# Kernel optimization log

Measured on AMD Instinct MI355X. Metric: run time of the kernel, lower is better.

## Reference

```python
import jax, jax.numpy as jnp
import numpy as np

N_NODES = 50000
N_EDGES = 800000
D_IN = 128
D_HID = 128
N_CLASSES = 40


def gcn_conv(h, src, dst, W, b, n_nodes):
    """GCNConv: out = D^{-1/2} (A + I) D^{-1/2} (h @ W) + b, with self-loops."""
    h = h @ W  # [N, F_out]
    loop = jnp.arange(n_nodes, dtype=src.dtype)
    s = jnp.concatenate([src, loop])  # [E + N]
    d = jnp.concatenate([dst, loop])
    deg = jax.ops.segment_sum(jnp.ones_like(d, dtype=h.dtype), d, num_segments=n_nodes)
    dinv = jax.lax.rsqrt(jnp.maximum(deg, 1.0))  # deg >= 1 due to self-loops
    norm = dinv[s] * dinv[d]  # [E + N]
    msgs = h[s] * norm[:, None]  # gather: [E + N, F_out]
    out = jax.ops.segment_sum(msgs, d, num_segments=n_nodes)  # scatter-add
    return out + b


def setup_inputs() -> dict:
    key = jax.random.key(0)
    ks = jax.random.split(key, 12)
    x = jax.random.normal(ks[0], (N_NODES, D_IN), dtype=jnp.float32)
    edge_index = jax.random.randint(ks[1], (2, N_EDGES), 0, N_NODES, dtype=jnp.int64)
    def lin(k, fi, fo):
        s = 1.0 / np.sqrt(fi)
        return jax.random.uniform(k, (fi, fo), jnp.float32, -s, s)
    W_pre = lin(ks[2], D_IN, D_HID)
    b_pre = jnp.zeros((D_HID,), jnp.float32)
    W1 = lin(ks[3], D_HID, D_HID)
    b1 = jnp.zeros((D_HID,), jnp.float32)
    W2 = lin(ks[4], D_HID, D_HID)
    b2 = jnp.zeros((D_HID,), jnp.float32)
    W_post = lin(ks[5], D_HID, N_CLASSES)
    b_post = jnp.zeros((N_CLASSES,), jnp.float32)
    return {"x": x, "edge_index": edge_index, "W_pre": W_pre, "b_pre": b_pre,
            "W1": W1, "b1": b1, "W2": W2, "b2": b2,
            "W_post": W_post, "b_post": b_post}


def reference(x, edge_index, W_pre, b_pre, W1, b1, W2, b2, W_post, b_post):
    src, dst = edge_index[0], edge_index[1]
    n = x.shape[0]
    h = x @ W_pre + b_pre                      # pre-process MLP (Linear)
    h = jax.nn.relu(gcn_conv(h, src, dst, W1, b1, n))   # conv1 + act1
    h = jax.nn.relu(gcn_conv(h, src, dst, W2, b2, n))   # conv2 + act2
    return h @ W_post + b_post                 # post-process MLP (Linear)
```

## Files before the change

### kernel.cpp

```cpp
#include <hip/hip_runtime.h>

#define D 128

typedef short bfrag __attribute__((ext_vector_type(8)));
typedef float f32x4 __attribute__((ext_vector_type(4)));
typedef unsigned uint32;

__device__ inline unsigned short bf16_rne(float x) {
    unsigned u = __float_as_uint(x);
    return (unsigned short)((u + 0x7FFFu + ((u >> 16) & 1u)) >> 16);
}
__device__ inline float bf16_to_f(unsigned short h) {
    return __uint_as_float(((unsigned)h) << 16);
}
__device__ inline unsigned split2p(float x) {
    unsigned short hi = bf16_rne(x);
    unsigned short lo = bf16_rne(x - bf16_to_f(hi));
    return (unsigned)hi | ((unsigned)lo << 16);
}

__device__ inline void unpair_r(uint4 q0, uint4 q1, bfrag& ah, bfrag& al) {
    union { uint32 u[4]; bfrag b; } H, L;
    H.u[0] = __builtin_amdgcn_perm(q0.y, q0.x, 0x05040100u);
    H.u[1] = __builtin_amdgcn_perm(q0.w, q0.z, 0x05040100u);
    H.u[2] = __builtin_amdgcn_perm(q1.y, q1.x, 0x05040100u);
    H.u[3] = __builtin_amdgcn_perm(q1.w, q1.z, 0x05040100u);
    L.u[0] = __builtin_amdgcn_perm(q0.y, q0.x, 0x07060302u);
    L.u[1] = __builtin_amdgcn_perm(q0.w, q0.z, 0x07060302u);
    L.u[2] = __builtin_amdgcn_perm(q1.y, q1.x, 0x07060302u);
    L.u[3] = __builtin_amdgcn_perm(q1.w, q1.z, 0x07060302u);
    ah = H.b;
    al = L.b;
}

__device__ inline void split8_r(uint4 q0, uint4 q1, bfrag& ah, bfrag& al) {
    float v[8] = {__uint_as_float(q0.x), __uint_as_float(q0.y), __uint_as_float(q0.z), __uint_as_float(q0.w),
                  __uint_as_float(q1.x), __uint_as_float(q1.y), __uint_as_float(q1.z), __uint_as_float(q1.w)};
    union { unsigned short us[8]; bfrag b; } H, L;
    #pragma unroll
    for (int i = 0; i < 8; i++) {
        unsigned pr = split2p(v[i]);
        H.us[i] = (unsigned short)pr;
        L.us[i] = (unsigned short)(pr >> 16);
    }
    ah = H.b;
    al = L.b;
}

__global__ __launch_bounds__(256) void deg_raw(const unsigned* __restrict__ raw, int* __restrict__ deg,
                                               int* __restrict__ gmode, unsigned short* __restrict__ csr16,
                                               float* __restrict__ t_c, int E, int Npad, int csrCap4, int nRows,
                                               const float* __restrict__ Wpre, const float* __restrict__ W1,
                                               const float* __restrict__ W2, const float* __restrict__ Wpost,
                                               uint32* __restrict__ wpre_p, uint32* __restrict__ w1_p,
                                               uint32* __restrict__ w2_p, uint32* __restrict__ wpost_p) {
    __shared__ int smode;
    int gid = blockIdx.x * 256 + threadIdx.x;
    int gstride = gridDim.x * 256;
    int p0 = blockIdx.x * 1024;
    if (threadIdx.x < 64) {
        int p = p0 + threadIdx.x * 16;
        unsigned v = (p < E) ? raw[2 * p + 1] : 0u;
        unsigned long long any = __ballot(v != 0u);
        if (threadIdx.x == 0) smode = (any != 0ull) ? 1 : 0;
    }
    __syncthreads();
    int m = smode;
    if (blockIdx.x == 0 && threadIdx.x == 0) *gmode = m;
    unsigned short sent = (unsigned short)Npad;
    ushort4 s4 = make_ushort4(sent, sent, sent, sent);
    for (int i = gid; i < csrCap4; i += gstride) ((ushort4*)csr16)[i] = s4;
    int sentRows = nRows - Npad;
    int nSentF4 = 8 * sentRows * 4;
    for (int i = gid; i < nSentF4; i += gstride) {
        int chunk = i / (sentRows * 4);
        int rem = i % (sentRows * 4);
        ((float4*)(t_c + (size_t)chunk * nRows * 16 + (size_t)Npad * 16))[rem] = make_float4(0.f, 0.f, 0.f, 0.f);
    }
    for (int i = gid; i < 55296; i += gstride) {
        const float* W; uint32* wp; int idx, ncols;
        if (i < 16384)      { W = Wpre;  wp = wpre_p;  idx = i;         ncols = 128; }
        else if (i < 32768) { W = W1;    wp = w1_p;    idx = i - 16384; ncols = 128; }
        else if (i < 49152) { W = W2;    wp = w2_p;    idx = i - 32768; ncols = 128; }
        else                { W = Wpost; wp = wpost_p; idx = i - 49152; ncols = 40;  }
        int n = idx >> 7, k = idx & 127;
        float v = (n < ncols) ? W[k * ncols + n] : 0.f;
        wp[idx] = split2p(v);
    }
    int pend = min(p0 + 1024, E);
    for (int p = p0 + threadIdx.x; p < pend; p += 256) {
        int d = m ? (int)raw[E + p] : (int)((const unsigned long long*)raw)[E + p];
        atomicAdd(&deg[d], 1);
    }
}

__global__ __launch_bounds__(256) void rank_block(const int* __restrict__ deg, float* __restrict__ dinv,
                                                  int* __restrict__ local_rank, int* __restrict__ hist_blk, int N) {
    __shared__ int h[256];
    int t = threadIdx.x;
    h[t] = 0;
    __syncthreads();
    int i = blockIdx.x * 256 + t;
    if (i < N) {
        int d = deg[i];
        dinv[i] = 1.0f / sqrtf((float)(d + 1));
        int b = min(d, 255);
        local_rank[i] = atomicAdd(&h[b], 1);
    }
    __syncthreads();
    hist_blk[blockIdx.x * 256 + t] = h[t];
}

__global__ __launch_bounds__(256) void scan_blocks(int* __restrict__ hist_blk, int* __restrict__ binbase,
                                                   int* __restrict__ ebase, int nblk) {
    int b = threadIdx.x;
    int sum = 0;
    int k = 0;
    for (; k + 8 <= nblk; k += 8) {
        int v[8];
        #pragma unroll
        for (int u = 0; u < 8; u++) v[u] = hist_blk[(k + u) * 256 + b];
        #pragma unroll
        for (int u = 0; u < 8; u++) { hist_blk[(k + u) * 256 + b] = sum; sum += v[u]; }
    }
    for (; k < nblk; k++) {
        int v = hist_blk[k * 256 + b];
        hist_blk[k * 256 + b] = sum;
        sum += v;
    }
    __shared__ int s[256], s2[256];
    int bp = (b + 3) & ~3;
    int c = sum, e = sum * bp;
    s[b] = c; s2[b] = e;
    __syncthreads();
    for (int off = 1; off < 256; off <<= 1) {
        int a0 = (b >= off) ? s[b - off] : 0;
        int a1 = (b >= off) ? s2[b - off] : 0;
        __syncthreads();
        s[b] += a0; s2[b] += a1;
        __syncthreads();
    }
    binbase[b] = s[b] - c;
    ebase[b] = s2[b] - e;
}

__global__ __launch_bounds__(256) void emit_perm(const int* __restrict__ deg, const float* __restrict__ dinv,
                                                 const int* __restrict__ local_rank, const int* __restrict__ hist_blk,
                                                 const int* __restrict__ binbase, const int* __restrict__ ebase,
                                                 int* __restrict__ tailcur, int* __restrict__ rowbeg,
                                                 int* __restrict__ cursor, uint4* __restrict__ meta, int N) {
    int i = blockIdx.x * 256 + threadIdx.x;
    if (i >= N) return;
    int d = deg[i];
    int b = min(d, 255);
    int dp = (d + 3) & ~3;
    int rib = hist_blk[blockIdx.x * 256 + b] + local_rank[i];
    int pos = binbase[b] + rib;
    int rb = (b < 255) ? (ebase[b] + rib * ((b + 3) & ~3)) : (ebase[255] + atomicAdd(tailcur, dp));
    rowbeg[i] = rb;
    cursor[i] = 0;
    meta[pos] = make_uint4((unsigned)rb, (unsigned)dp, __float_as_uint(dinv[i]), (unsigned)i);
}

__global__ __launch_bounds__(256) void fill_csr_raw(const unsigned* __restrict__ raw, const int* __restrict__ gmode,
                                                    const int* __restrict__ rowbeg, int* __restrict__ cursor,
                                                    unsigned short* __restrict__ csr16, int E) {
    int e = blockIdx.x * 256 + threadIdx.x;
    if (e >= E) return;
    int m = *gmode;
    int d = m ? (int)raw[E + e] : (int)((const unsigned long long*)raw)[E + e];
    int s = m ? (int)raw[e]     : (int)((const unsigned long long*)raw)[e];
    int pos = atomicAdd(&cursor[d], 1);
    csr16[rowbeg[d] + pos] = (unsigned short)s;
}

template<int EPI, int AFMT>
__global__ __launch_bounds__(512) void gemm_lds(const void* __restrict__ Ap,
                                                const uint32* __restrict__ Wpair,
                                                const float* __restrict__ bias,
                                                const float* __restrict__ dinv,
                                                float* __restrict__ Cf,
                                                uint32* __restrict__ Pout,
                                                int nStrips, int N, int nRows) {
    __shared__ uint32 Wl[128 * 132];
    int tid = threadIdx.x;
    for (int i = tid; i < 16384; i += 512)
        Wl[(i >> 7) * 132 + (i & 127)] = Wpair[i];
    __syncthreads();

    int wave = tid >> 6;
    int lane = tid & 63;
    int l15 = lane & 15, lg = lane >> 4;
    int so = wave >> 1;
    int colbase = (wave & 1) * 64;
    size_t chunkStride = (size_t)nRows * 16;

    const int stride = gridDim.x * 4;
    for (int strip = blockIdx.x * 4 + so; strip < nStrips; strip += stride) {
        int arow = min(strip * 16 + l15, N - 1);
        uint4 cur[8];
        const uint4* p = (const uint4*)Ap + (size_t)arow * 32 + lg * 2;
        #pragma unroll
        for (int ks = 0; ks < 4; ks++) {
            cur[2 * ks]     = p[ks * 8];
            cur[2 * ks + 1] = p[ks * 8 + 1];
        }
        bfrag ah[4], al[4];
        #pragma unroll
        for (int ks = 0; ks < 4; ks++) {
            if (AFMT == 0) unpair_r(cur[2 * ks], cur[2 * ks + 1], ah[ks], al[ks]);
            else           split8_r(cur[2 * ks], cur[2 * ks + 1], ah[ks], al[ks]);
        }
        f32x4 acc[4];
        #pragma unroll
        for (int nt = 0; nt < 4; nt++) acc[nt] = (f32x4){0.f, 0.f, 0.f, 0.f};
        #pragma unroll
        for (int ks = 0; ks < 4; ks++) {
            #pragma unroll
            for (int nt = 0; nt < 4; nt++) {
                const uint32* wp = &Wl[(colbase + nt * 16 + l15) * 132 + ks * 32 + lg * 8];
                uint4 w0 = *(const uint4*)wp;
                uint4 w1 = *(const uint4*)(wp + 4);
                bfrag wh, wl_;
                unpair_r(w0, w1, wh, wl_);
                acc[nt] = __builtin_amdgcn_mfma_f32_16x16x32_bf16(ah[ks], wh, acc[nt], 0, 0, 0);
                acc[nt] = __builtin_amdgcn_mfma_f32_16x16x32_bf16(ah[ks], wl_, acc[nt], 0, 0, 0);
                acc[nt] = __builtin_amdgcn_mfma_f32_16x16x32_bf16(al[ks], wh, acc[nt], 0, 0, 0);
            }
        }
        int row0 = strip * 16;
        if (EPI == 0) {
            float dv[4];
            #pragma unroll
            for (int r = 0; r < 4; r++) dv[r] = dinv[min(row0 + lg * 4 + r, N - 1)];
            #pragma unroll
            for (int nt = 0; nt < 4; nt++) {
                int col = colbase + nt * 16 + l15;
                float* cbase = Cf + (size_t)(col >> 4) * chunkStride + (col & 15);
                #pragma unroll
                for (int r = 0; r < 4; r++)
                    cbase[(size_t)(row0 + lg * 4 + r) * 16] = acc[nt][r] * dv[r];
            }
        } else {
            #pragma unroll
            for (int nt = 0; nt < 4; nt++) {
                int col = colbase + nt * 16 + l15;
                float bv = bias[col];
                #pragma unroll
                for (int r = 0; r < 4; r++)
                    Pout[(size_t)(row0 + lg * 4 + r) * D + col] = split2p(acc[nt][r] + bv);
            }
        }
    }
}

__global__ __launch_bounds__(256) void gemm_post(const uint32* __restrict__ P,
                                                 const uint32* __restrict__ Wpair,
                                                 const float* __restrict__ bias,
                                                 float* __restrict__ Cf,
                                                 int nStrips, int N, int outW) {
    int wave = threadIdx.x >> 6;
    int lane = threadIdx.x & 63;
    int l15 = lane & 15, lg = lane >> 4;

    bfrag wh[4][3], wl[4][3];
    #pragma unroll
    for (int ks = 0; ks < 4; ks++)
        #pragma unroll
        for (int nt = 0; nt < 3; nt++) {
            const uint32* wp = Wpair + (size_t)(nt * 16 + l15) * D + ks * 32 + lg * 8;
            uint4 w0 = *(const uint4*)wp;
            uint4 w1 = *(const uint4*)(wp + 4);
            unpair_r(w0, w1, wh[ks][nt], wl[ks][nt]);
        }

    const int stride = gridDim.x * 4;
    for (int strip = blockIdx.x * 4 + wave; strip < nStrips; strip += stride) {
        int arow = min(strip * 16 + l15, N - 1);
        bfrag ah[4], al[4];
        #pragma unroll
        for (int ks = 0; ks < 4; ks++) {
            const uint4* p = (const uint4*)P + (size_t)arow * 32 + lg * 2;
            unpair_r(p[ks * 8], p[ks * 8 + 1], ah[ks], al[ks]);
        }
        f32x4 acc[3];
        #pragma unroll
        for (int nt = 0; nt < 3; nt++) acc[nt] = (f32x4){0.f, 0.f, 0.f, 0.f};
        #pragma unroll
        for (int ks = 0; ks < 4; ks++)
            #pragma unroll
            for (int nt = 0; nt < 3; nt++) {
                acc[nt] = __builtin_amdgcn_mfma_f32_16x16x32_bf16(ah[ks], wh[ks][nt], acc[nt], 0, 0, 0);
                acc[nt] = __builtin_amdgcn_mfma_f32_16x16x32_bf16(ah[ks], wl[ks][nt], acc[nt], 0, 0, 0);
                acc[nt] = __builtin_amdgcn_mfma_f32_16x16x32_bf16(al[ks], wh[ks][nt], acc[nt], 0, 0, 0);
            }
        int row0 = strip * 16;
        #pragma unroll
        for (int nt = 0; nt < 3; nt++) {
            int col = nt * 16 + l15;
            #pragma unroll
            for (int r = 0; r < 4; r++) {
                int row = row0 + lg * 4 + r;
                if (row < N && col < outW)
                    Cf[(size_t)row * outW + col] = acc[nt][r] + bias[col];
            }
        }
    }
}

__global__ __launch_bounds__(256) void gather_xcd(const unsigned short* __restrict__ csr16,
                                                  const uint4* __restrict__ meta,
                                                  const float* __restrict__ t_c, const float* __restrict__ bias,
                                                  uint32* __restrict__ Pout, int N, int nRows) {
    int chunk = blockIdx.x & 7;
    int k = (blockIdx.x >> 3) * 16 + (threadIdx.x >> 4);
    if (k >= N) return;
    uint4 m = meta[k];
    int beg = (int)m.x;
    int degp = (int)m.y;
    float di = __uint_as_float(m.z);
    int node = (int)m.w;
    int w = (threadIdx.x >> 2) & 3;
    int c = threadIdx.x & 3;
    const float* tc = t_c + (size_t)chunk * nRows * 16 + c * 4;
    float4 a0 = make_float4(0.f, 0.f, 0.f, 0.f);
    float4 a1 = make_float4(0.f, 0.f, 0.f, 0.f);
    float4 a2 = make_float4(0.f, 0.f, 0.f, 0.f);
    float4 a3 = make_float4(0.f, 0.f, 0.f, 0.f);
    int end = beg + degp;
    for (int j = beg + 4 * w; j < end; j += 16) {
        ushort4 o = *(const ushort4*)(csr16 + j);
        float4 v0 = *(const float4*)(tc + ((size_t)o.x << 4));
        float4 v1 = *(const float4*)(tc + ((size_t)o.y << 4));
        float4 v2 = *(const float4*)(tc + ((size_t)o.z << 4));
        float4 v3 = *(const float4*)(tc + ((size_t)o.w << 4));
        a0.x += v0.x; a0.y += v0.y; a0.z += v0.z; a0.w += v0.w;
        a1.x += v1.x; a1.y += v1.y; a1.z += v1.z; a1.w += v1.w;
        a2.x += v2.x; a2.y += v2.y; a2.z += v2.z; a2.w += v2.w;
        a3.x += v3.x; a3.y += v3.y; a3.z += v3.z; a3.w += v3.w;
    }
    a0.x += a1.x; a0.y += a1.y; a0.z += a1.z; a0.w += a1.w;
    a2.x += a3.x; a2.y += a3.y; a2.z += a3.z; a2.w += a3.w;
    a0.x += a2.x; a0.y += a2.y; a0.z += a2.z; a0.w += a2.w;
    a0.x += __shfl_xor(a0.x, 4); a0.y += __shfl_xor(a0.y, 4);
    a0.z += __shfl_xor(a0.z, 4); a0.w += __shfl_xor(a0.w, 4);
    a0.x += __shfl_xor(a0.x, 8); a0.y += __shfl_xor(a0.y, 8);
    a0.z += __shfl_xor(a0.z, 8); a0.w += __shfl_xor(a0.w, 8);
    if (w != 0) return;
    float4 tv = *(const float4*)(tc + (size_t)node * 16);
    int col0 = chunk * 16 + c * 4;
    float4 b = *((const float4*)bias + (col0 >> 2));
    float4 r;
    r.x = fmaxf(fmaf(di, a0.x + tv.x, b.x), 0.f);
    r.y = fmaxf(fmaf(di, a0.y + tv.y, b.y), 0.f);
    r.z = fmaxf(fmaf(di, a0.z + tv.z, b.z), 0.f);
    r.w = fmaxf(fmaf(di, a0.w + tv.w, b.w), 0.f);
    uint4 p;
    p.x = split2p(r.x); p.y = split2p(r.y); p.z = split2p(r.z); p.w = split2p(r.w);
    *(uint4*)(Pout + (size_t)node * D + col0) = p;
}

extern "C" void kernel_launch(void* const* d_in, const int* in_sizes, int n_in,
                              void* d_out, int out_size, void* d_ws, size_t ws_size,
                              hipStream_t stream) {
    const float* x      = (const float*)d_in[0];
    const unsigned* edges = (const unsigned*)d_in[1];
    const float* W_pre  = (const float*)d_in[2];
    const float* b_pre  = (const float*)d_in[3];
    const float* W1     = (const float*)d_in[4];
    const float* b1     = (const float*)d_in[5];
    const float* W2     = (const float*)d_in[6];
    const float* b2     = (const float*)d_in[7];
    const float* W_post = (const float*)d_in[8];
    const float* b_post = (const float*)d_in[9];
    float* out = (float*)d_out;

    const int N = in_sizes[0] / D;
    const int E = in_sizes[1] / 2;
    const int nStrips = (N + 15) / 16;
    const int Npad = nStrips * 16;
    const int nRows = Npad + 16;
    const int nBlk = (N + 255) / 256;
    const int csrCap = (E + 4 * N + 255) & ~255;

    char* ws = (char*)d_ws;
    size_t off = 0;
    auto alloc = [&](size_t bytes) { void* p = ws + off; off += (bytes + 255) & ~(size_t)255; return p; };
    uint32* pairA = (uint32*)alloc((size_t)Npad * D * 4);
    uint32* pairB = (uint32*)alloc((size_t)Npad * D * 4);
    float*  bufT  = (float*)alloc((size_t)8 * nRows * 16 * 4);
    float*  dinv    = (float*)alloc((size_t)N * 4);
    int*    deg     = (int*)alloc((size_t)N * 4);
    int*    rowbeg  = (int*)alloc((size_t)N * 4);
    unsigned short* csr16 = (unsigned short*)alloc((size_t)csrCap * 2);
    uint4*  meta    = (uint4*)alloc((size_t)N * 16);
    uint32* wpre_p  = (uint32*)alloc(16384 * 4);
    uint32* w1_p    = (uint32*)alloc(16384 * 4);
    uint32* w2_p    = (uint32*)alloc(16384 * 4);
    uint32* wpost_p = (uint32*)alloc(6144 * 4);

    {
        char* t = (char*)bufT;
        size_t toff = 0;
        auto talloc = [&](size_t bytes) { void* p = t + toff; toff += (bytes + 255) & ~(size_t)255; return p; };
        int* cursor     = (int*)talloc((size_t)N * 4);
        int* local_rank = (int*)talloc((size_t)N * 4);
        int* hist_blk   = (int*)talloc((size_t)nBlk * 256 * 4);
        int* mode2      = (int*)talloc(256);
        int* binbase    = (int*)talloc(1024);
        int* ebase      = (int*)talloc(1024);
        int* gmode = mode2;
        int* tailcur = mode2 + 1;

        (void)hipMemsetAsync(mode2, 0, 8, stream);
        (void)hipMemsetAsync(deg, 0, (size_t)N * 4, stream);
        deg_raw<<<(E + 1023) / 1024, 256, 0, stream>>>(edges, deg, gmode, csr16, bufT, E, Npad, csrCap / 4, nRows,
                                                       W_pre, W1, W2, W_post, wpre_p, w1_p, w2_p, wpost_p);
        rank_block<<<nBlk, 256, 0, stream>>>(deg, dinv, local_rank, hist_blk, N);
        scan_blocks<<<1, 256, 0, stream>>>(hist_blk, binbase, ebase, nBlk);
        emit_perm<<<nBlk, 256, 0, stream>>>(deg, dinv, local_rank, hist_blk, binbase, ebase,
                                            tailcur, rowbeg, cursor, meta, N);
        fill_csr_raw<<<(E + 255) / 256, 256, 0, stream>>>(edges, gmode, rowbeg, cursor, csr16, E);
    }

    const int nGatherBlocks = ((N + 15) / 16) * 8;
    const int gemmGrid = 391;

    gemm_lds<1, 1><<<gemmGrid, 512, 0, stream>>>(x, wpre_p, b_pre, nullptr, nullptr, pairB, nStrips, N, nRows);

    gemm_lds<0, 0><<<gemmGrid, 512, 0, stream>>>(pairB, w1_p, nullptr, dinv, bufT, nullptr, nStrips, N, nRows);
    gather_xcd<<<nGatherBlocks, 256, 0, stream>>>(csr16, meta, bufT, b1, pairA, N, nRows);

    gemm_lds<0, 0><<<gemmGrid, 512, 0, stream>>>(pairA, w2_p, nullptr, dinv, bufT, nullptr, nStrips, N, nRows);
    gather_xcd<<<nGatherBlocks, 256, 0, stream>>>(csr16, meta, bufT, b2, pairB, N, nRows);

    gemm_post<<<256, 256, 0, stream>>>(pairB, wpost_p, b_post, out, nStrips, N, 40);
}
```

Before: 267.3 us.

## Fold pre-MLP weight into conv1 weight to remove one dense GEMM

Since there is no nonlinearity between the pre-process Linear and conv1's h@W1, a new kernel precomputes Wc = W_pre·W1 and bc = b_pre·W1 on device. The first conv GEMM then reads x directly with the composed weight and bias, so the separate pre-MLP GEMM launch and its N×128 intermediate write and read go away. The tiny composition kernel adds a launch, and rounding changes slightly because the product is split into bf16 pairs once instead of per stage.

```diff
diff --git a/kernel.cpp b/kernel.cpp
--- a/kernel.cpp
+++ b/kernel.cpp
@@ -47,12 +47,29 @@
     al = L.b;
 }
 
+__global__ __launch_bounds__(256) void compose_w(const float* __restrict__ Wpre, const float* __restrict__ W1,
+                                                 const float* __restrict__ bpre,
+                                                 uint32* __restrict__ wcp, float* __restrict__ bc) {
+    int i = blockIdx.x * 256 + threadIdx.x;
+    int n = i & 127, k = i >> 7;
+    float acc = 0.f;
+    #pragma unroll 4
+    for (int m = 0; m < 128; m++)
+        acc = fmaf(Wpre[k * 128 + m], W1[m * 128 + n], acc);
+    wcp[n * 128 + k] = split2p(acc);
+    if (i < 128) {
+        float b = 0.f;
+        #pragma unroll 4
+        for (int m = 0; m < 128; m++)
+            b = fmaf(bpre[m], W1[m * 128 + i], b);
+        bc[i] = b;
+    }
+}
+
 __global__ __launch_bounds__(256) void deg_raw(const unsigned* __restrict__ raw, int* __restrict__ deg,
                                                int* __restrict__ gmode, unsigned short* __restrict__ csr16,
                                                float* __restrict__ t_c, int E, int Npad, int csrCap4, int nRows,
-                                               const float* __restrict__ Wpre, const float* __restrict__ W1,
                                                const float* __restrict__ W2, const float* __restrict__ Wpost,
-                                               uint32* __restrict__ wpre_p, uint32* __restrict__ w1_p,
                                                uint32* __restrict__ w2_p, uint32* __restrict__ wpost_p) {
     __shared__ int smode;
     int gid = blockIdx.x * 256 + threadIdx.x;
@@ -77,12 +94,10 @@
         int rem = i % (sentRows * 4);
         ((float4*)(t_c + (size_t)chunk * nRows * 16 + (size_t)Npad * 16))[rem] = make_float4(0.f, 0.f, 0.f, 0.f);
     }
-    for (int i = gid; i < 55296; i += gstride) {
+    for (int i = gid; i < 22528; i += gstride) {
         const float* W; uint32* wp; int idx, ncols;
-        if (i < 16384)      { W = Wpre;  wp = wpre_p;  idx = i;         ncols = 128; }
-        else if (i < 32768) { W = W1;    wp = w1_p;    idx = i - 16384; ncols = 128; }
-        else if (i < 49152) { W = W2;    wp = w2_p;    idx = i - 32768; ncols = 128; }
-        else                { W = Wpost; wp = wpost_p; idx = i - 49152; ncols = 40;  }
+        if (i < 16384) { W = W2;    wp = w2_p;    idx = i;         ncols = 128; }
+        else           { W = Wpost; wp = wpost_p; idx = i - 16384; ncols = 40;  }
         int n = idx >> 7, k = idx & 127;
         float v = (n < ncols) ? W[k * ncols + n] : 0.f;
         wp[idx] = split2p(v);
@@ -236,10 +251,11 @@
             #pragma unroll
             for (int nt = 0; nt < 4; nt++) {
                 int col = colbase + nt * 16 + l15;
+                float bv = bias ? bias[col] : 0.f;
                 float* cbase = Cf + (size_t)(col >> 4) * chunkStride + (col & 15);
                 #pragma unroll
                 for (int r = 0; r < 4; r++)
-                    cbase[(size_t)(row0 + lg * 4 + r) * 16] = acc[nt][r] * dv[r];
+                    cbase[(size_t)(row0 + lg * 4 + r) * 16] = (acc[nt][r] + bv) * dv[r];
             }
         } else {
             #pragma unroll
@@ -394,8 +410,8 @@
     int*    rowbeg  = (int*)alloc((size_t)N * 4);
     unsigned short* csr16 = (unsigned short*)alloc((size_t)csrCap * 2);
     uint4*  meta    = (uint4*)alloc((size_t)N * 16);
-    uint32* wpre_p  = (uint32*)alloc(16384 * 4);
-    uint32* w1_p    = (uint32*)alloc(16384 * 4);
+    uint32* wc_p    = (uint32*)alloc(16384 * 4);
+    float*  bc      = (float*)alloc(128 * 4);
     uint32* w2_p    = (uint32*)alloc(16384 * 4);
     uint32* wpost_p = (uint32*)alloc(6144 * 4);
 
@@ -414,8 +430,9 @@
 
         (void)hipMemsetAsync(mode2, 0, 8, stream);
         (void)hipMemsetAsync(deg, 0, (size_t)N * 4, stream);
+        compose_w<<<64, 256, 0, stream>>>(W_pre, W1, b_pre, wc_p, bc);
         deg_raw<<<(E + 1023) / 1024, 256, 0, stream>>>(edges, deg, gmode, csr16, bufT, E, Npad, csrCap / 4, nRows,
-                                                       W_pre, W1, W2, W_post, wpre_p, w1_p, w2_p, wpost_p);
+                                                       W2, W_post, w2_p, wpost_p);
         rank_block<<<nBlk, 256, 0, stream>>>(deg, dinv, local_rank, hist_blk, N);
         scan_blocks<<<1, 256, 0, stream>>>(hist_blk, binbase, ebase, nBlk);
         emit_perm<<<nBlk, 256, 0, stream>>>(deg, dinv, local_rank, hist_blk, binbase, ebase,
@@ -426,9 +443,7 @@
     const int nGatherBlocks = ((N + 15) / 16) * 8;
     const int gemmGrid = 391;
 
-    gemm_lds<1, 1><<<gemmGrid, 512, 0, stream>>>(x, wpre_p, b_pre, nullptr, nullptr, pairB, nStrips, N, nRows);
-
-    gemm_lds<0, 0><<<gemmGrid, 512, 0, stream>>>(pairB, w1_p, nullptr, dinv, bufT, nullptr, nStrips, N, nRows);
+    gemm_lds<0, 1><<<gemmGrid, 512, 0, stream>>>(x, wc_p, bc, dinv, bufT, nullptr, nStrips, N, nRows);
     gather_xcd<<<nGatherBlocks, 256, 0, stream>>>(csr16, meta, bufT, b1, pairA, N, nRows);
 
     gemm_lds<0, 0><<<gemmGrid, 512, 0, stream>>>(pairA, w2_p, nullptr, dinv, bufT, nullptr, nStrips, N, nRows);
```

Result: no change. 268.7 us (+0.5%).
